# Kernel tuning notes

Measured on AMD Instinct MI355X. Metric: run time of the kernel, lower is better.

The kernel has to match this reference:

```python
import jax
import jax.numpy as jnp
from jax import lax
import numpy as np

# Module constants (from init_kwargs)
SCALE = 2
CIN = 256
COUT = 256
KER = 3
R = 4
CMID = CIN // R
PAD = KER // 2          # ConvTranspose2d padding
OUT_PAD = SCALE - 1     # ConvTranspose2d output_padding

B, H, W = 4, 64, 64
HO, WO = H * SCALE, W * SCALE


def conv_transpose2d(x, w, b, stride, padding, output_padding):
    """PyTorch ConvTranspose2d. x: [B,Cin,H,W], w: [Cin,Cout,k,k] (torch layout)."""
    k = w.shape[2]
    # rot180 + swap in/out channels -> regular conv kernel [Cout,Cin,k,k]
    wr = jnp.transpose(jnp.flip(w, (2, 3)), (1, 0, 2, 3))
    pad = (k - 1 - padding, k - 1 - padding + output_padding)
    y = lax.conv_general_dilated(
        x, wr, window_strides=(1, 1), padding=[pad, pad],
        lhs_dilation=(stride, stride),
        dimension_numbers=('NCHW', 'OIHW', 'NCHW'))
    return y + b[None, :, None, None]


def setup_inputs() -> dict:
    key = jax.random.key(0)
    k1, k2, k3, k4, k5 = jax.random.split(key, 5)
    inx = jax.random.normal(k1, (B, CIN, H, W), dtype=jnp.float32)
    mask = jax.random.bernoulli(k2, 0.5, (B, 1, HO, WO)).astype(jnp.float32)
    inv_mask = 1.0 - mask
    # params, initialized per the module's init scheme
    w_high = 0.001 * jax.random.normal(k3, (CIN, COUT, KER, KER), dtype=jnp.float32)
    b_high = jnp.zeros((COUT,), dtype=jnp.float32)
    std1 = float(np.sqrt(2.0 / (CMID * 1 * 1)))
    w_low1 = std1 * jax.random.normal(k4, (CMID, CIN, 1, 1), dtype=jnp.float32)
    b_low1 = jnp.zeros((CMID,), dtype=jnp.float32)
    w_low2 = 0.001 * jax.random.normal(k5, (CMID, COUT, KER, KER), dtype=jnp.float32)
    b_low2 = jnp.zeros((COUT,), dtype=jnp.float32)
    return {"inx": inx, "mask": mask, "inv_mask": inv_mask,
            "w_high": w_high, "b_high": b_high,
            "w_low1": w_low1, "b_low1": b_low1,
            "w_low2": w_low2, "b_low2": b_low2}


def reference(inx, mask, inv_mask, w_high, b_high, w_low1, b_low1, w_low2, b_low2):
    # high branch: full-rank transposed conv, routed by mask
    x1 = conv_transpose2d(inx, w_high, b_high, SCALE, PAD, OUT_PAD) * mask
    # low branch: 1x1 bottleneck then transposed conv, routed by inv_mask
    x2 = jnp.einsum('bchw,oc->bohw', inx, w_low1[:, :, 0, 0]) + b_low1[None, :, None, None]
    x2 = conv_transpose2d(x2, w_low2, b_low2, SCALE, PAD, OUT_PAD) * inv_mask
    return x1 + x2
```

## Files before the change

### kernel.cpp

```cpp
#include <hip/hip_runtime.h>
#include <cstdint>
#include <cstddef>

#define CIN   256
#define COUT  256
#define CMID  64
#define H     64
#define W     64
#define HO    128
#define WO    128
#define BATCH 4

typedef unsigned short u16;
typedef unsigned int   u32;
typedef __attribute__((ext_vector_type(8))) __bf16 bf16x8;
typedef __attribute__((ext_vector_type(4))) float f32x4;

#define XT_ROW  16384
#define X2_ROW  4096

#define AS1 __attribute__((address_space(1)))
#define AS3 __attribute__((address_space(3)))

__device__ __forceinline__ void g2l16(const void* g, const void* l) {
    __builtin_amdgcn_global_load_lds((const AS1 u32*)(uintptr_t)g,
                                     (AS3 u32*)(u32)(uintptr_t)l, 16, 0, 0);
}

__device__ __forceinline__ u16 f2bf(float f) {
    u32 u = __builtin_bit_cast(u32, f);
    u += 0x7fffu + ((u >> 16) & 1u);
    return (u16)(u >> 16);
}

__global__ __launch_bounds__(256) void k_pack_w(const float* __restrict__ wH,
                                                const float* __restrict__ wL,
                                                const float* __restrict__ w1,
                                                u16* __restrict__ WPH,
                                                u16* __restrict__ WPL,
                                                u16* __restrict__ W1P) {
    const int t = blockIdx.x / 8;
    const int kc = blockIdx.x % 8;
    const int co = threadIdx.x;
    #pragma unroll
    for (int q = 0; q < 4; ++q) {
        u16 pk[8];
        #pragma unroll
        for (int j = 0; j < 8; ++j) {
            int ci = kc * 32 + q * 8 + j;
            pk[j] = f2bf(wH[((size_t)ci * COUT + co) * 9 + t]);
        }
        *(ushort4*)(WPH + ((((size_t)t * 8 + kc) * 4 + q) * 256 + co) * 8)     = *(ushort4*)&pk[0];
        *(ushort4*)(WPH + ((((size_t)t * 8 + kc) * 4 + q) * 256 + co) * 8 + 4) = *(ushort4*)&pk[4];
    }
    if (kc < 2) {
        #pragma unroll
        for (int q = 0; q < 4; ++q) {
            u16 pk[8];
            #pragma unroll
            for (int j = 0; j < 8; ++j) {
                int cm = kc * 32 + q * 8 + j;
                pk[j] = f2bf(wL[((size_t)cm * COUT + co) * 9 + t]);
            }
            *(ushort4*)(WPL + ((((size_t)t * 2 + kc) * 4 + q) * 256 + co) * 8)     = *(ushort4*)&pk[0];
            *(ushort4*)(WPL + ((((size_t)t * 2 + kc) * 4 + q) * 256 + co) * 8 + 4) = *(ushort4*)&pk[4];
        }
    }
    if (t == 0 && co < CMID) {
        #pragma unroll
        for (int q = 0; q < 4; ++q) {
            u16 pk[8];
            #pragma unroll
            for (int j = 0; j < 8; ++j)
                pk[j] = f2bf(w1[(size_t)co * CIN + kc * 32 + q * 8 + j]);
            *(ushort4*)(W1P + (((size_t)kc * 4 + q) * 64 + co) * 8)     = *(ushort4*)&pk[0];
            *(ushort4*)(W1P + (((size_t)kc * 4 + q) * 64 + co) * 8 + 4) = *(ushort4*)&pk[4];
        }
    }
}

__global__ __launch_bounds__(256) void k_prep(const float* __restrict__ inx,
                                              const u16* __restrict__ W1P,
                                              const float* __restrict__ b1,
                                              u16* __restrict__ Xt,
                                              u16* __restrict__ X2t) {
    __shared__ u16 sX[32 * 64 * 8];
    const int b = blockIdx.x / 65;
    const int y = blockIdx.x % 65;
    const int tid = threadIdx.x;
    u16* xrow  = Xt  + (size_t)(b * 65 + y) * XT_ROW;
    u16* x2row = X2t + (size_t)(b * 65 + y) * X2_ROW;
    if (y == H) {
        uint4 z = {0, 0, 0, 0};
        #pragma unroll
        for (int i = 0; i < 8; ++i) *(uint4*)(xrow + (i * 256 + tid) * 8) = z;
        #pragma unroll
        for (int i = 0; i < 2; ++i) *(uint4*)(x2row + (i * 256 + tid) * 8) = z;
        return;
    }
    const int x = tid & 63, g0 = tid >> 6;
    #pragma unroll
    for (int gg = 0; gg < 8; ++gg) {
        const int s = gg * 4 + g0;
        u16 pk[8];
        #pragma unroll
        for (int j = 0; j < 8; ++j)
            pk[j] = f2bf(inx[(((size_t)b * CIN + s * 8 + j) * H + y) * W + x]);
        uint4 v = *(uint4*)pk;
        *(uint4*)(xrow + ((size_t)s * 64 + x) * 8) = v;
        *(uint4*)(sX   + ((size_t)s * 64 + x) * 8) = v;
    }
    __syncthreads();
    const int wv = tid >> 6, lane = tid & 63, l15 = lane & 15, q = lane >> 4;
    f32x4 acc[4] = {};
    #pragma unroll
    for (int kc = 0; kc < 8; ++kc) {
        bf16x8 bfr = *(const bf16x8*)(sX + ((size_t)(kc * 4 + q) * 64 + wv * 16 + l15) * 8);
        #pragma unroll
        for (int mi = 0; mi < 4; ++mi) {
            bf16x8 af = *(const bf16x8*)(W1P + (((size_t)kc * 4 + q) * 64 + mi * 16 + l15) * 8);
            acc[mi] = __builtin_amdgcn_mfma_f32_16x16x32_bf16(af, bfr, acc[mi], 0, 0, 0);
        }
    }
    const int xx = wv * 16 + l15;
    #pragma unroll
    for (int mi = 0; mi < 4; ++mi) {
        const int kc2 = mi >> 1;
        const int qq  = ((mi & 1) << 1) | (q >> 1);
        u16 pk[4];
        #pragma unroll
        for (int r = 0; r < 4; ++r)
            pk[r] = f2bf(acc[mi][r] + b1[mi * 16 + q * 4 + r]);
        *(ushort4*)(x2row + ((size_t)(kc2 * 4 + qq) * 64 + xx) * 8 + (q & 1) * 4) = *(ushort4*)&pk[0];
    }
}

__global__ __launch_bounds__(256, 2) void k_main(const u16* __restrict__ Xt,
                                                 const u16* __restrict__ X2t,
                                                 const u16* __restrict__ WPH,
                                                 const u16* __restrict__ WPL,
                                                 const float* __restrict__ bH,
                                                 const float* __restrict__ bL,
                                                 const float* __restrict__ mask,
                                                 float* __restrict__ out) {
    __shared__ u16 sA[2 * 3 * 4 * 128 * 8];
    __shared__ u16 sB[3 * 4 * 65 * 8];

    const int blk = blockIdx.x;
    const int coH = blk & 1;
    const int yP  = (blk >> 1) & 31;
    const int b   = (blk >> 6) & 3;
    const int py  = blk >> 8;
    const int y0  = yP * 2;
    const int nr  = py + 1;

    const int tid = threadIdx.x;
    const int wid = tid >> 6, lane = tid & 63, l15 = lane & 15, q = lane >> 4;
    const int rowR = wid >> 1, coQ = wid & 1;
    const int oy = 2 * (y0 + rowR) + py;

    int selE[4], selO[4];
    const float* mrow = mask + ((size_t)b * HO + oy) * WO;
    #pragma unroll
    for (int ni = 0; ni < 4; ++ni) {
        float2 mm = *(const float2*)(mrow + 2 * (ni * 16 + l15));
        selE[ni] = (mm.x != 0.f);
        selO[ni] = (mm.y != 0.f);
    }

    if (tid < 12) {
        uint4 z = {0, 0, 0, 0};
        *(uint4*)(sB + (((tid >> 2) * 4 + (tid & 3)) * 65 + 64) * 8) = z;
    }

    f32x4 ce[4][4] = {}, co_[4][4] = {};

    for (int c = 0; c < 10; ++c) {
        const bool hi = (c < 8);
        const int hiI = hi ? 1 : 0;
        const int kc  = hi ? c : c - 8;
        const int kcn = hi ? 8 : 2;
        const u16* Wp = hi ? WPH : WPL;
        const u16* Xp = hi ? Xt : X2t;
        const size_t rowStr = hi ? XT_ROW : X2_ROW;

        __syncthreads();
        for (int dy = 0; dy < nr; ++dy) {
            const int ky = py ? (dy ? 0 : 2) : 1;
            #pragma unroll
            for (int s = 0; s < 6; ++s) {
                const int seg = s * 4 + wid;
                const int h = seg & 1, qq = (seg >> 1) & 3, kx = seg >> 3;
                const u16* src = Wp + ((((size_t)(ky * 3 + kx) * kcn + kc) * 4 + qq) * 256
                                        + coH * 128 + h * 64 + lane) * 8;
                const u16* dst = sA + ((((size_t)(dy * 3 + kx) * 4 + qq) * 128 + h * 64)) * 8;
                g2l16(src, dst);
            }
        }
        for (int r = 0; r <= nr; ++r) {
            const u16* src = Xp + (size_t)(b * 65 + y0 + r) * rowStr
                                + ((size_t)(kc * 4 + wid) * 64 + lane) * 8;
            const u16* dst = sB + ((size_t)(r * 4 + wid) * 65) * 8;
            g2l16(src, dst);
        }
        __syncthreads();

        for (int dy = 0; dy < nr; ++dy) {
            const int rB = rowR + dy;
            const u16* bp = sB + (((size_t)(rB * 4 + q)) * 65 + l15) * 8;
            bf16x8 b0[4], b1[4];
            #pragma unroll
            for (int ni = 0; ni < 4; ++ni) {
                b0[ni] = *(const bf16x8*)(bp + (size_t)ni * 16 * 8);
                b1[ni] = *(const bf16x8*)(bp + ((size_t)ni * 16 + 1) * 8);
            }
            const bf16x8 z8 = {};
            bf16x8 be[4], bo0[4], bo1[4];
            #pragma unroll
            for (int ni = 0; ni < 4; ++ni) {
                be[ni]  = (selE[ni] == hiI) ? b0[ni] : z8;
                bo0[ni] = (selO[ni] == hiI) ? b0[ni] : z8;
                bo1[ni] = (selO[ni] == hiI) ? b1[ni] : z8;
            }
            const u16* ap = sA + ((size_t)dy * 1536 + q * 128 + coQ * 64 + l15) * 8;
            bf16x8 a[4];
            #pragma unroll
            for (int mi = 0; mi < 4; ++mi) a[mi] = *(const bf16x8*)(ap + ((size_t)1 * 512 + mi * 16) * 8);
            #pragma unroll
            for (int mi = 0; mi < 4; ++mi)
                #pragma unroll
                for (int ni = 0; ni < 4; ++ni)
                    ce[mi][ni] = __builtin_amdgcn_mfma_f32_16x16x32_bf16(a[mi], be[ni], ce[mi][ni], 0, 0, 0);
            #pragma unroll
            for (int mi = 0; mi < 4; ++mi) a[mi] = *(const bf16x8*)(ap + ((size_t)2 * 512 + mi * 16) * 8);
            #pragma unroll
            for (int mi = 0; mi < 4; ++mi)
                #pragma unroll
                for (int ni = 0; ni < 4; ++ni)
                    co_[mi][ni] = __builtin_amdgcn_mfma_f32_16x16x32_bf16(a[mi], bo0[ni], co_[mi][ni], 0, 0, 0);
            #pragma unroll
            for (int mi = 0; mi < 4; ++mi) a[mi] = *(const bf16x8*)(ap + ((size_t)mi * 16) * 8);
            #pragma unroll
            for (int mi = 0; mi < 4; ++mi)
                #pragma unroll
                for (int ni = 0; ni < 4; ++ni)
                    co_[mi][ni] = __builtin_amdgcn_mfma_f32_16x16x32_bf16(a[mi], bo1[ni], co_[mi][ni], 0, 0, 0);
        }
    }

    #pragma unroll
    for (int mi = 0; mi < 4; ++mi) {
        const int cob = coH * 128 + coQ * 64 + mi * 16 + q * 4;
        float bh[4], bl[4];
        #pragma unroll
        for (int r = 0; r < 4; ++r) { bh[r] = bH[cob + r]; bl[r] = bL[cob + r]; }
        #pragma unroll
        for (int r = 0; r < 4; ++r) {
            float* orow = out + (((size_t)b * COUT + cob + r) * HO + oy) * WO;
            #pragma unroll
            for (int ni = 0; ni < 4; ++ni) {
                const int x = ni * 16 + l15;
                float2 v;
                v.x = ce[mi][ni][r]  + (selE[ni] ? bh[r] : bl[r]);
                v.y = co_[mi][ni][r] + (selO[ni] ? bh[r] : bl[r]);
                *(float2*)(orow + 2 * x) = v;
            }
        }
    }
}

extern "C" void kernel_launch(void* const* d_in, const int* in_sizes, int n_in,
                              void* d_out, int out_size, void* d_ws, size_t ws_size,
                              hipStream_t stream) {
    const float* inx    = (const float*)d_in[0];
    const float* mask   = (const float*)d_in[1];
    const float* w_high = (const float*)d_in[3];
    const float* b_high = (const float*)d_in[4];
    const float* w_low1 = (const float*)d_in[5];
    const float* b_low1 = (const float*)d_in[6];
    const float* w_low2 = (const float*)d_in[7];
    const float* b_low2 = (const float*)d_in[8];
    float* out = (float*)d_out;

    char* ws = (char*)d_ws;
    u16* Xt  = (u16*)(ws);
    u16* X2t = (u16*)(ws + 8519680);
    u16* WPH = (u16*)(ws + 10649600);
    u16* WPL = (u16*)(ws + 11829248);
    u16* W1P = (u16*)(ws + 12124160);

    k_pack_w<<<72, 256, 0, stream>>>(w_high, w_low2, w_low1, WPH, WPL, W1P);
    k_prep<<<BATCH * 65, 256, 0, stream>>>(inx, W1P, b_low1, Xt, X2t);
    k_main<<<512, 256, 0, stream>>>(Xt, X2t, WPH, WPL, b_high, b_low2, mask, out);
}
```

Before: 133.9 us.

## Drop LDS staging in main kernel and merge weight packing into prep kernel

The main kernel no longer stages weights and input rows through LDS with barriers. Each wave now reads its MFMA operands directly from global memory (relying on L1/L2 caching), using a row layout padded to 65 columns so the x+1 halo is available in place. Weight packing is folded into the prep kernel as extra blocks, with the 1x1 weights converted into LDS per block, which saves one launch. The change trades LDS traffic and syncs for many more global/L2 loads and longer load latency in the inner loop.

```diff
diff --git a/kernel.cpp b/kernel.cpp
--- a/kernel.cpp
+++ b/kernel.cpp
@@ -16,16 +16,8 @@
 typedef __attribute__((ext_vector_type(8))) __bf16 bf16x8;
 typedef __attribute__((ext_vector_type(4))) float f32x4;
 
-#define XT_ROW  16384
-#define X2_ROW  4096
-
-#define AS1 __attribute__((address_space(1)))
-#define AS3 __attribute__((address_space(3)))
-
-__device__ __forceinline__ void g2l16(const void* g, const void* l) {
-    __builtin_amdgcn_global_load_lds((const AS1 u32*)(uintptr_t)g,
-                                     (AS3 u32*)(u32)(uintptr_t)l, 16, 0, 0);
-}
+#define XT_ROW  16640
+#define X2_ROW  4160
 
 __device__ __forceinline__ u16 f2bf(float f) {
     u32 u = __builtin_bit_cast(u32, f);
@@ -33,71 +25,71 @@
     return (u16)(u >> 16);
 }
 
-__global__ __launch_bounds__(256) void k_pack_w(const float* __restrict__ wH,
-                                                const float* __restrict__ wL,
-                                                const float* __restrict__ w1,
-                                                u16* __restrict__ WPH,
-                                                u16* __restrict__ WPL,
-                                                u16* __restrict__ W1P) {
-    const int t = blockIdx.x / 8;
-    const int kc = blockIdx.x % 8;
-    const int co = threadIdx.x;
-    #pragma unroll
-    for (int q = 0; q < 4; ++q) {
-        u16 pk[8];
-        #pragma unroll
-        for (int j = 0; j < 8; ++j) {
-            int ci = kc * 32 + q * 8 + j;
-            pk[j] = f2bf(wH[((size_t)ci * COUT + co) * 9 + t]);
-        }
-        *(ushort4*)(WPH + ((((size_t)t * 8 + kc) * 4 + q) * 256 + co) * 8)     = *(ushort4*)&pk[0];
-        *(ushort4*)(WPH + ((((size_t)t * 8 + kc) * 4 + q) * 256 + co) * 8 + 4) = *(ushort4*)&pk[4];
-    }
-    if (kc < 2) {
+__global__ __launch_bounds__(256) void k_prep(const float* __restrict__ inx,
+                                              const float* __restrict__ w1,
+                                              const float* __restrict__ b1,
+                                              const float* __restrict__ wH,
+                                              const float* __restrict__ wL,
+                                              u16* __restrict__ Xt,
+                                              u16* __restrict__ X2t,
+                                              u16* __restrict__ WPH,
+                                              u16* __restrict__ WPL) {
+    __shared__ u16 sX[32 * 64 * 8];
+    __shared__ u16 sW1[8 * 4 * 64 * 8];
+    const int blk = blockIdx.x;
+    const int tid = threadIdx.x;
+
+    if (blk >= BATCH * 65) {
+        const int pb = blk - BATCH * 65;
+        const int t = pb / 8;
+        const int kc = pb % 8;
+        const int co = tid;
         #pragma unroll
         for (int q = 0; q < 4; ++q) {
             u16 pk[8];
             #pragma unroll
             for (int j = 0; j < 8; ++j) {
-                int cm = kc * 32 + q * 8 + j;
-                pk[j] = f2bf(wL[((size_t)cm * COUT + co) * 9 + t]);
-            }
-            *(ushort4*)(WPL + ((((size_t)t * 2 + kc) * 4 + q) * 256 + co) * 8)     = *(ushort4*)&pk[0];
-            *(ushort4*)(WPL + ((((size_t)t * 2 + kc) * 4 + q) * 256 + co) * 8 + 4) = *(ushort4*)&pk[4];
-        }
-    }
-    if (t == 0 && co < CMID) {
-        #pragma unroll
-        for (int q = 0; q < 4; ++q) {
-            u16 pk[8];
-            #pragma unroll
-            for (int j = 0; j < 8; ++j)
-                pk[j] = f2bf(w1[(size_t)co * CIN + kc * 32 + q * 8 + j]);
-            *(ushort4*)(W1P + (((size_t)kc * 4 + q) * 64 + co) * 8)     = *(ushort4*)&pk[0];
-            *(ushort4*)(W1P + (((size_t)kc * 4 + q) * 64 + co) * 8 + 4) = *(ushort4*)&pk[4];
-        }
-    }
-}
-
-__global__ __launch_bounds__(256) void k_prep(const float* __restrict__ inx,
-                                              const u16* __restrict__ W1P,
-                                              const float* __restrict__ b1,
-                                              u16* __restrict__ Xt,
-                                              u16* __restrict__ X2t) {
-    __shared__ u16 sX[32 * 64 * 8];
-    const int b = blockIdx.x / 65;
-    const int y = blockIdx.x % 65;
-    const int tid = threadIdx.x;
+                int ci = kc * 32 + q * 8 + j;
+                pk[j] = f2bf(wH[((size_t)ci * COUT + co) * 9 + t]);
+            }
+            *(uint4*)(WPH + ((((size_t)t * 8 + kc) * 4 + q) * 256 + co) * 8) = *(uint4*)pk;
+        }
+        if (kc < 2) {
+            #pragma unroll
+            for (int q = 0; q < 4; ++q) {
+                u16 pk[8];
+                #pragma unroll
+                for (int j = 0; j < 8; ++j) {
+                    int cm = kc * 32 + q * 8 + j;
+                    pk[j] = f2bf(wL[((size_t)cm * COUT + co) * 9 + t]);
+                }
+                *(uint4*)(WPL + ((((size_t)t * 2 + kc) * 4 + q) * 256 + co) * 8) = *(uint4*)pk;
+            }
+        }
+        return;
+    }
+
+    const int b = blk / 65;
+    const int y = blk % 65;
     u16* xrow  = Xt  + (size_t)(b * 65 + y) * XT_ROW;
     u16* x2row = X2t + (size_t)(b * 65 + y) * X2_ROW;
     if (y == H) {
         uint4 z = {0, 0, 0, 0};
-        #pragma unroll
-        for (int i = 0; i < 8; ++i) *(uint4*)(xrow + (i * 256 + tid) * 8) = z;
-        #pragma unroll
-        for (int i = 0; i < 2; ++i) *(uint4*)(x2row + (i * 256 + tid) * 8) = z;
+        for (int i = tid; i < XT_ROW / 8; i += 256) *(uint4*)(xrow + i * 8) = z;
+        for (int i = tid; i < X2_ROW / 8; i += 256) *(uint4*)(x2row + i * 8) = z;
         return;
     }
+
+    #pragma unroll
+    for (int i = 0; i < 16; ++i) {
+        int lin4 = i * 256 + tid;
+        float4 v = ((const float4*)w1)[lin4];
+        int lin = lin4 * 4;
+        int cm = lin >> 8, ci = lin & 255;
+        u16* dp = sW1 + (((size_t)(ci >> 3) * 64 + cm) * 8) + (ci & 7);
+        dp[0] = f2bf(v.x); dp[1] = f2bf(v.y); dp[2] = f2bf(v.z); dp[3] = f2bf(v.w);
+    }
+
     const int x = tid & 63, g0 = tid >> 6;
     #pragma unroll
     for (int gg = 0; gg < 8; ++gg) {
@@ -107,10 +99,19 @@
         for (int j = 0; j < 8; ++j)
             pk[j] = f2bf(inx[(((size_t)b * CIN + s * 8 + j) * H + y) * W + x]);
         uint4 v = *(uint4*)pk;
-        *(uint4*)(xrow + ((size_t)s * 64 + x) * 8) = v;
+        *(uint4*)(xrow + ((size_t)s * 65 + x) * 8) = v;
         *(uint4*)(sX   + ((size_t)s * 64 + x) * 8) = v;
     }
+    if (tid < 32) {
+        uint4 z = {0, 0, 0, 0};
+        *(uint4*)(xrow + ((size_t)tid * 65 + 64) * 8) = z;
+    }
+    if (tid < 8) {
+        uint4 z = {0, 0, 0, 0};
+        *(uint4*)(x2row + ((size_t)tid * 65 + 64) * 8) = z;
+    }
     __syncthreads();
+
     const int wv = tid >> 6, lane = tid & 63, l15 = lane & 15, q = lane >> 4;
     f32x4 acc[4] = {};
     #pragma unroll
@@ -118,20 +119,112 @@
         bf16x8 bfr = *(const bf16x8*)(sX + ((size_t)(kc * 4 + q) * 64 + wv * 16 + l15) * 8);
         #pragma unroll
         for (int mi = 0; mi < 4; ++mi) {
-            bf16x8 af = *(const bf16x8*)(W1P + (((size_t)kc * 4 + q) * 64 + mi * 16 + l15) * 8);
+            bf16x8 af = *(const bf16x8*)(sW1 + (((size_t)kc * 4 + q) * 64 + mi * 16 + l15) * 8);
             acc[mi] = __builtin_amdgcn_mfma_f32_16x16x32_bf16(af, bfr, acc[mi], 0, 0, 0);
         }
     }
     const int xx = wv * 16 + l15;
     #pragma unroll
     for (int mi = 0; mi < 4; ++mi) {
-        const int kc2 = mi >> 1;
-        const int qq  = ((mi & 1) << 1) | (q >> 1);
+        const int s = mi * 2 + (q >> 1);
         u16 pk[4];
         #pragma unroll
         for (int r = 0; r < 4; ++r)
             pk[r] = f2bf(acc[mi][r] + b1[mi * 16 + q * 4 + r]);
-        *(ushort4*)(x2row + ((size_t)(kc2 * 4 + qq) * 64 + xx) * 8 + (q & 1) * 4) = *(ushort4*)&pk[0];
+        *(ushort4*)(x2row + ((size_t)s * 65 + xx) * 8 + (q & 1) * 4) = *(ushort4*)&pk[0];
+    }
+}
+
+template<int NR>
+__device__ __forceinline__ void accum_all(const u16* __restrict__ Xt,
+                                          const u16* __restrict__ X2t,
+                                          const u16* __restrict__ WPH,
+                                          const u16* __restrict__ WPL,
+                                          int b, int y0, int rowR, int coLane,
+                                          int q, int l15,
+                                          const int* __restrict__ selE,
+                                          const int* __restrict__ selO,
+                                          f32x4 ce[4][4], f32x4 co_[4][4]) {
+    const bf16x8 z8 = {};
+    #pragma unroll 2
+    for (int kc = 0; kc < 8; ++kc) {
+        #pragma unroll
+        for (int dy = 0; dy < NR; ++dy) {
+            const int ky = (NR == 1) ? 1 : (dy ? 0 : 2);
+            const u16* bp = Xt + (size_t)(b * 65 + y0 + rowR + dy) * XT_ROW
+                               + ((size_t)(kc * 4 + q) * 65 + l15) * 8;
+            bf16x8 be[4], bo0[4], bo1[4];
+            #pragma unroll
+            for (int ni = 0; ni < 4; ++ni) {
+                bf16x8 b0 = *(const bf16x8*)(bp + ni * 128);
+                bf16x8 b1 = *(const bf16x8*)(bp + ni * 128 + 8);
+                be[ni]  = selE[ni] ? b0 : z8;
+                bo0[ni] = selO[ni] ? b0 : z8;
+                bo1[ni] = selO[ni] ? b1 : z8;
+            }
+            const u16* ap = WPH + ((((size_t)(ky * 3) * 8 + kc) * 4 + q) * 256 + coLane) * 8;
+            #pragma unroll
+            for (int mi = 0; mi < 4; ++mi) {
+                bf16x8 a = *(const bf16x8*)(ap + 65536 + mi * 128);
+                #pragma unroll
+                for (int ni = 0; ni < 4; ++ni)
+                    ce[mi][ni] = __builtin_amdgcn_mfma_f32_16x16x32_bf16(a, be[ni], ce[mi][ni], 0, 0, 0);
+            }
+            #pragma unroll
+            for (int mi = 0; mi < 4; ++mi) {
+                bf16x8 a = *(const bf16x8*)(ap + 131072 + mi * 128);
+                #pragma unroll
+                for (int ni = 0; ni < 4; ++ni)
+                    co_[mi][ni] = __builtin_amdgcn_mfma_f32_16x16x32_bf16(a, bo0[ni], co_[mi][ni], 0, 0, 0);
+            }
+            #pragma unroll
+            for (int mi = 0; mi < 4; ++mi) {
+                bf16x8 a = *(const bf16x8*)(ap + mi * 128);
+                #pragma unroll
+                for (int ni = 0; ni < 4; ++ni)
+                    co_[mi][ni] = __builtin_amdgcn_mfma_f32_16x16x32_bf16(a, bo1[ni], co_[mi][ni], 0, 0, 0);
+            }
+        }
+    }
+    #pragma unroll
+    for (int kc = 0; kc < 2; ++kc) {
+        #pragma unroll
+        for (int dy = 0; dy < NR; ++dy) {
+            const int ky = (NR == 1) ? 1 : (dy ? 0 : 2);
+            const u16* bp = X2t + (size_t)(b * 65 + y0 + rowR + dy) * X2_ROW
+                                + ((size_t)(kc * 4 + q) * 65 + l15) * 8;
+            bf16x8 be[4], bo0[4], bo1[4];
+            #pragma unroll
+            for (int ni = 0; ni < 4; ++ni) {
+                bf16x8 b0 = *(const bf16x8*)(bp + ni * 128);
+                bf16x8 b1 = *(const bf16x8*)(bp + ni * 128 + 8);
+                be[ni]  = selE[ni] ? z8 : b0;
+                bo0[ni] = selO[ni] ? z8 : b0;
+                bo1[ni] = selO[ni] ? z8 : b1;
+            }
+            const u16* ap = WPL + ((((size_t)(ky * 3) * 2 + kc) * 4 + q) * 256 + coLane) * 8;
+            #pragma unroll
+            for (int mi = 0; mi < 4; ++mi) {
+                bf16x8 a = *(const bf16x8*)(ap + 16384 + mi * 128);
+                #pragma unroll
+                for (int ni = 0; ni < 4; ++ni)
+                    ce[mi][ni] = __builtin_amdgcn_mfma_f32_16x16x32_bf16(a, be[ni], ce[mi][ni], 0, 0, 0);
+            }
+            #pragma unroll
+            for (int mi = 0; mi < 4; ++mi) {
+                bf16x8 a = *(const bf16x8*)(ap + 32768 + mi * 128);
+                #pragma unroll
+                for (int ni = 0; ni < 4; ++ni)
+                    co_[mi][ni] = __builtin_amdgcn_mfma_f32_16x16x32_bf16(a, bo0[ni], co_[mi][ni], 0, 0, 0);
+            }
+            #pragma unroll
+            for (int mi = 0; mi < 4; ++mi) {
+                bf16x8 a = *(const bf16x8*)(ap + mi * 128);
+                #pragma unroll
+                for (int ni = 0; ni < 4; ++ni)
+                    co_[mi][ni] = __builtin_amdgcn_mfma_f32_16x16x32_bf16(a, bo1[ni], co_[mi][ni], 0, 0, 0);
+            }
+        }
     }
 }
 
@@ -143,21 +236,18 @@
                                                  const float* __restrict__ bL,
                                                  const float* __restrict__ mask,
                                                  float* __restrict__ out) {
-    __shared__ u16 sA[2 * 3 * 4 * 128 * 8];
-    __shared__ u16 sB[3 * 4 * 65 * 8];
-
     const int blk = blockIdx.x;
     const int coH = blk & 1;
     const int yP  = (blk >> 1) & 31;
     const int b   = (blk >> 6) & 3;
     const int py  = blk >> 8;
     const int y0  = yP * 2;
-    const int nr  = py + 1;
 
     const int tid = threadIdx.x;
     const int wid = tid >> 6, lane = tid & 63, l15 = lane & 15, q = lane >> 4;
     const int rowR = wid >> 1, coQ = wid & 1;
     const int oy = 2 * (y0 + rowR) + py;
+    const int coLane = coH * 128 + coQ * 64 + l15;
 
     int selE[4], selO[4];
     const float* mrow = mask + ((size_t)b * HO + oy) * WO;
@@ -168,85 +258,11 @@
         selO[ni] = (mm.y != 0.f);
     }
 
-    if (tid < 12) {
-        uint4 z = {0, 0, 0, 0};
-        *(uint4*)(sB + (((tid >> 2) * 4 + (tid & 3)) * 65 + 64) * 8) = z;
-    }
-
     f32x4 ce[4][4] = {}, co_[4][4] = {};
-
-    for (int c = 0; c < 10; ++c) {
-        const bool hi = (c < 8);
-        const int hiI = hi ? 1 : 0;
-        const int kc  = hi ? c : c - 8;
-        const int kcn = hi ? 8 : 2;
-        const u16* Wp = hi ? WPH : WPL;
-        const u16* Xp = hi ? Xt : X2t;
-        const size_t rowStr = hi ? XT_ROW : X2_ROW;
-
-        __syncthreads();
-        for (int dy = 0; dy < nr; ++dy) {
-            const int ky = py ? (dy ? 0 : 2) : 1;
-            #pragma unroll
-            for (int s = 0; s < 6; ++s) {
-                const int seg = s * 4 + wid;
-                const int h = seg & 1, qq = (seg >> 1) & 3, kx = seg >> 3;
-                const u16* src = Wp + ((((size_t)(ky * 3 + kx) * kcn + kc) * 4 + qq) * 256
-                                        + coH * 128 + h * 64 + lane) * 8;
-                const u16* dst = sA + ((((size_t)(dy * 3 + kx) * 4 + qq) * 128 + h * 64)) * 8;
-                g2l16(src, dst);
-            }
-        }
-        for (int r = 0; r <= nr; ++r) {
-            const u16* src = Xp + (size_t)(b * 65 + y0 + r) * rowStr
-                                + ((size_t)(kc * 4 + wid) * 64 + lane) * 8;
-            const u16* dst = sB + ((size_t)(r * 4 + wid) * 65) * 8;
-            g2l16(src, dst);
-        }
-        __syncthreads();
-
-        for (int dy = 0; dy < nr; ++dy) {
-            const int rB = rowR + dy;
-            const u16* bp = sB + (((size_t)(rB * 4 + q)) * 65 + l15) * 8;
-            bf16x8 b0[4], b1[4];
-            #pragma unroll
-            for (int ni = 0; ni < 4; ++ni) {
-                b0[ni] = *(const bf16x8*)(bp + (size_t)ni * 16 * 8);
-                b1[ni] = *(const bf16x8*)(bp + ((size_t)ni * 16 + 1) * 8);
-            }
-            const bf16x8 z8 = {};
-            bf16x8 be[4], bo0[4], bo1[4];
-            #pragma unroll
-            for (int ni = 0; ni < 4; ++ni) {
-                be[ni]  = (selE[ni] == hiI) ? b0[ni] : z8;
-                bo0[ni] = (selO[ni] == hiI) ? b0[ni] : z8;
-                bo1[ni] = (selO[ni] == hiI) ? b1[ni] : z8;
-            }
-            const u16* ap = sA + ((size_t)dy * 1536 + q * 128 + coQ * 64 + l15) * 8;
-            bf16x8 a[4];
-            #pragma unroll
-            for (int mi = 0; mi < 4; ++mi) a[mi] = *(const bf16x8*)(ap + ((size_t)1 * 512 + mi * 16) * 8);
-            #pragma unroll
-            for (int mi = 0; mi < 4; ++mi)
-                #pragma unroll
-                for (int ni = 0; ni < 4; ++ni)
-                    ce[mi][ni] = __builtin_amdgcn_mfma_f32_16x16x32_bf16(a[mi], be[ni], ce[mi][ni], 0, 0, 0);
-            #pragma unroll
-            for (int mi = 0; mi < 4; ++mi) a[mi] = *(const bf16x8*)(ap + ((size_t)2 * 512 + mi * 16) * 8);
-            #pragma unroll
-            for (int mi = 0; mi < 4; ++mi)
-                #pragma unroll
-                for (int ni = 0; ni < 4; ++ni)
-                    co_[mi][ni] = __builtin_amdgcn_mfma_f32_16x16x32_bf16(a[mi], bo0[ni], co_[mi][ni], 0, 0, 0);
-            #pragma unroll
-            for (int mi = 0; mi < 4; ++mi) a[mi] = *(const bf16x8*)(ap + ((size_t)mi * 16) * 8);
-            #pragma unroll
-            for (int mi = 0; mi < 4; ++mi)
-                #pragma unroll
-                for (int ni = 0; ni < 4; ++ni)
-                    co_[mi][ni] = __builtin_amdgcn_mfma_f32_16x16x32_bf16(a[mi], bo1[ni], co_[mi][ni], 0, 0, 0);
-        }
-    }
+    if (py == 0)
+        accum_all<1>(Xt, X2t, WPH, WPL, b, y0, rowR, coLane, q, l15, selE, selO, ce, co_);
+    else
+        accum_all<2>(Xt, X2t, WPH, WPL, b, y0, rowR, coLane, q, l15, selE, selO, ce, co_);
 
     #pragma unroll
     for (int mi = 0; mi < 4; ++mi) {
@@ -284,12 +300,11 @@
 
     char* ws = (char*)d_ws;
     u16* Xt  = (u16*)(ws);
-    u16* X2t = (u16*)(ws + 8519680);
-    u16* WPH = (u16*)(ws + 10649600);
-    u16* WPL = (u16*)(ws + 11829248);
-    u16* W1P = (u16*)(ws + 12124160);
-
-    k_pack_w<<<72, 256, 0, stream>>>(w_high, w_low2, w_low1, WPH, WPL, W1P);
-    k_prep<<<BATCH * 65, 256, 0, stream>>>(inx, W1P, b_low1, Xt, X2t);
+    u16* X2t = (u16*)(ws + 8652800);
+    u16* WPH = (u16*)(ws + 10816000);
+    u16* WPL = (u16*)(ws + 11995648);
+
+    k_prep<<<BATCH * 65 + 72, 256, 0, stream>>>(inx, w_low1, b_low1, w_high, w_low2,
+                                                Xt, X2t, WPH, WPL);
     k_main<<<512, 256, 0, stream>>>(Xt, X2t, WPH, WPL, b_high, b_low2, mask, out);
 }
```

New measurement: 144.4 us. 1.08x slower.
